# Performance work log

Hardware: AMD Instinct MI355X
Metric: run time of the kernel (lower is better)

## Reference

```python
import jax, jax.numpy as jnp
import numpy as np


def setup_inputs() -> dict:
    key = jax.random.key(0)
    ks = jax.random.split(key, 6)
    B, Tq, Tk = 4, 512, 512
    Q, K, C = 1024, 1024, 256
    query = jax.random.normal(ks[0], (B, Tq, Q), dtype=jnp.float32)
    kmat = jax.random.normal(ks[1], (B, Tk, K), dtype=jnp.float32)
    # Linear weights (torch nn.Linear stores [out, in]; we keep [in, out] for einsum)
    Wq = jax.random.normal(ks[2], (Q, C), dtype=jnp.float32) / np.sqrt(Q)
    Wk = jax.random.normal(ks[3], (K, C), dtype=jnp.float32) / np.sqrt(K)
    w_attn = jax.random.normal(ks[4], (C,), dtype=jnp.float32) / np.sqrt(C)
    b_attn = jax.random.normal(ks[5], (), dtype=jnp.float32) * 0.01
    return {"query": query, "key": kmat, "Wq": Wq, "Wk": Wk,
            "w_attn": w_attn, "b_attn": b_attn}


def reference(query, key, Wq, Wk, w_attn, b_attn):
    # Additive (Bahdanau) attention scores.
    # q2ctx: (B, Tq, C); k2ctx: (B, Tk, C)
    q2ctx = jnp.einsum('bqi,ic->bqc', query, Wq)
    k2ctx = jnp.einsum('bki,ic->bkc', key, Wk)
    # broadcast add -> (B, Tq, Tk, C), tanh, project to scalar and squeeze
    ctx = jnp.tanh(q2ctx[:, :, None, :] + k2ctx[:, None, :, :])
    scores = jnp.einsum('bqkc,c->bqk', ctx, w_attn) + b_attn
    return scores  # (B, Tq, Tk)
```

## Files before the change

### kernel.cpp

```cpp
#include <hip/hip_runtime.h>
#include <hip/hip_bf16.h>

#define M_ROWS 2048
#define KDIM   1024
#define CDIM   256
#define TQ     512
#define TK     512

#define GBM 64
#define GBN 32
#define CK  128

#define SCALE2LOG2E 2.8853900817779268f

typedef __attribute__((ext_vector_type(8))) short short8;
typedef __attribute__((ext_vector_type(8))) unsigned short ushort8;
typedef __attribute__((ext_vector_type(4))) float floatx4;
typedef __attribute__((ext_vector_type(2))) float f32x2;

__device__ __forceinline__ short2 cvt2(float x, float y) {
    __hip_bfloat162 h = __float22bfloat162_rn(make_float2(x, y));
    short2 r;
    __builtin_memcpy(&r, &h, sizeof(r));
    return r;
}
__device__ __forceinline__ unsigned short f2bf1(float x) {
    return (unsigned short)cvt2(x, x).x;
}
__device__ __forceinline__ float bf2f(unsigned short u) {
    return __builtin_bit_cast(float, (unsigned)u << 16);
}
__device__ __forceinline__ f32x2 splat2(float x) { return (f32x2){x, x}; }

__global__ __launch_bounds__(256) void gemm_mfma_kernel(
    const float* __restrict__ Aq, const float* __restrict__ Ak,
    const float* __restrict__ Wq, const float* __restrict__ Wk,
    const float* __restrict__ w_attn,
    unsigned short* __restrict__ Eq, unsigned short* __restrict__ Ek)
{
    __shared__ short Ws[GBN][CK + 8];

    const int z = blockIdx.z;
    const float* A = z ? Ak : Aq;
    const float* W = z ? Wk : Wq;
    unsigned short* E = z ? Ek : Eq;

    const int t    = threadIdx.x;
    const int lane = t & 63;
    const int wave = t >> 6;
    const int m0   = blockIdx.x * GBM;
    const int n0   = blockIdx.y * GBN;
    const int li   = lane & 15;
    const int qd   = lane >> 4;

    const int row = m0 + wave * 16 + li;
    const float* Arow = A + (size_t)row * KDIM + qd * 8;

    const int kr = t >> 1;
    const int h  = t & 1;
    const float* Wst = W + (size_t)kr * CDIM + n0 + h * 16;

    floatx4 acc0 = {0.f, 0.f, 0.f, 0.f};
    floatx4 acc1 = {0.f, 0.f, 0.f, 0.f};

    float4 wreg[4];
    #pragma unroll
    for (int u = 0; u < 4; ++u) wreg[u] = *(const float4*)&Wst[4 * u];

    for (int ck = 0; ck < KDIM / CK; ++ck) {
        __syncthreads();
        #pragma unroll
        for (int u = 0; u < 4; ++u) {
            short2 e0 = cvt2(wreg[u].x, wreg[u].y);
            short2 e1 = cvt2(wreg[u].z, wreg[u].w);
            const int c = h * 16 + 4 * u;
            Ws[c + 0][kr] = e0.x;
            Ws[c + 1][kr] = e0.y;
            Ws[c + 2][kr] = e1.x;
            Ws[c + 3][kr] = e1.y;
        }
        __syncthreads();
        if (ck + 1 < KDIM / CK) {
            const float* Wn = Wst + (size_t)(ck + 1) * CK * CDIM;
            #pragma unroll
            for (int u = 0; u < 4; ++u) wreg[u] = *(const float4*)&Wn[4 * u];
        }
        #pragma unroll
        for (int s = 0; s < 4; ++s) {
            const int kk = ck * CK + s * 32;
            float4 a0 = *(const float4*)&Arow[kk];
            float4 a1 = *(const float4*)&Arow[kk + 4];
            short8 af0 = *(const short8*)&Ws[li][s * 32 + qd * 8];
            short8 af1 = *(const short8*)&Ws[16 + li][s * 32 + qd * 8];
            short2 p0 = cvt2(a0.x, a0.y), p1 = cvt2(a0.z, a0.w);
            short2 p2 = cvt2(a1.x, a1.y), p3 = cvt2(a1.z, a1.w);
            short8 bv = { p0.x, p0.y, p1.x, p1.y, p2.x, p2.y, p3.x, p3.y };
            acc0 = __builtin_amdgcn_mfma_f32_16x16x32_bf16(af0, bv, acc0, 0, 0, 0);
            acc1 = __builtin_amdgcn_mfma_f32_16x16x32_bf16(af1, bv, acc1, 0, 0, 0);
        }
    }

    #pragma unroll
    for (int r = 0; r < 4; ++r) {
        const int c0 = n0 + qd * 4 + r;
        const int c1 = c0 + 16;
        float s0 = z ? 1.0f : (-0.5f / w_attn[c0]);
        float s1 = z ? 1.0f : (-0.5f / w_attn[c1]);
        float v0 = __builtin_amdgcn_exp2f(acc0[r] * SCALE2LOG2E) * s0;
        float v1 = __builtin_amdgcn_exp2f(acc1[r] * SCALE2LOG2E) * s1;
        E[(size_t)c0 * M_ROWS + row] = f2bf1(v0);
        E[(size_t)c1 * M_ROWS + row] = f2bf1(v1);
    }
}

__global__ __launch_bounds__(256) void bahdanau_kernel(
    const unsigned short* __restrict__ Eqs, const unsigned short* __restrict__ Ek,
    const float* __restrict__ w_attn, const float* __restrict__ b_attn,
    float* __restrict__ out)
{
    __shared__ float qs[64][36];
    __shared__ float ks[64][36];
    __shared__ __align__(16) float sl[CDIM];
    __shared__ float partial[4];

    const int t  = threadIdx.x;
    const int b  = blockIdx.z;
    const int q0 = blockIdx.x * 32;
    const int k0 = blockIdx.y * 32;
    const int gq = b * TQ + q0;
    const int gk = b * TK + k0;
    const int tq = (t >> 4) * 2;
    const int tk = (t & 15) * 2;

    const int lr = t >> 2;
    const int lc = (t & 3) * 8;

    {
        float wv = w_attn[t];
        sl[t] = -0.5f / wv;
        float sum = wv;
        #pragma unroll
        for (int o = 32; o >= 1; o >>= 1) sum += __shfl_down(sum, o);
        if ((t & 63) == 0) partial[t >> 6] = sum;
    }

    ushort8 qu = *(const ushort8*)&Eqs[(size_t)lr * M_ROWS + gq + lc];
    ushort8 ku = *(const ushort8*)&Ek [(size_t)lr * M_ROWS + gk + lc];

    f32x2 accA = {0.f, 0.f};
    f32x2 accB = {0.f, 0.f};

    for (int ch = 0; ch < 4; ++ch) {
        __syncthreads();
        *(float4*)&qs[lr][lc]     = make_float4(bf2f(qu[0]), bf2f(qu[1]), bf2f(qu[2]), bf2f(qu[3]));
        *(float4*)&qs[lr][lc + 4] = make_float4(bf2f(qu[4]), bf2f(qu[5]), bf2f(qu[6]), bf2f(qu[7]));
        *(float4*)&ks[lr][lc]     = make_float4(bf2f(ku[0]), bf2f(ku[1]), bf2f(ku[2]), bf2f(ku[3]));
        *(float4*)&ks[lr][lc + 4] = make_float4(bf2f(ku[4]), bf2f(ku[5]), bf2f(ku[6]), bf2f(ku[7]));
        __syncthreads();
        if (ch < 3) {
            const int c1 = (ch + 1) * 64;
            qu = *(const ushort8*)&Eqs[(size_t)(c1 + lr) * M_ROWS + gq + lc];
            ku = *(const ushort8*)&Ek [(size_t)(c1 + lr) * M_ROWS + gk + lc];
        }
        const int cb = ch * 64;
        #pragma unroll
        for (int cc = 0; cc < 64; cc += 4) {
            float4 s4 = *(const float4*)&sl[cb + cc];
            f32x2 q1 = *(const f32x2*)&qs[cc + 0][tq];
            f32x2 q2 = *(const f32x2*)&qs[cc + 1][tq];
            f32x2 q3 = *(const f32x2*)&qs[cc + 2][tq];
            f32x2 q4 = *(const f32x2*)&qs[cc + 3][tq];
            f32x2 k1 = *(const f32x2*)&ks[cc + 0][tk];
            f32x2 k2 = *(const f32x2*)&ks[cc + 1][tk];
            f32x2 k3 = *(const f32x2*)&ks[cc + 2][tk];
            f32x2 k4 = *(const f32x2*)&ks[cc + 3][tk];
            {
                f32x2 f1 = __builtin_elementwise_fma(splat2(q1.x), k1, splat2(s4.x));
                f32x2 f2 = __builtin_elementwise_fma(splat2(q2.x), k2, splat2(s4.y));
                f32x2 f3 = __builtin_elementwise_fma(splat2(q3.x), k3, splat2(s4.z));
                f32x2 f4 = __builtin_elementwise_fma(splat2(q4.x), k4, splat2(s4.w));
                f32x2 p12 = f1 * f2, p34 = f3 * f4;
                f32x2 s12 = f1 + f2, s34 = f3 + f4;
                f32x2 num = __builtin_elementwise_fma(s12, p34, s34 * p12);
                f32x2 den = p12 * p34;
                f32x2 r = {__builtin_amdgcn_rcpf(den.x), __builtin_amdgcn_rcpf(den.y)};
                accA = __builtin_elementwise_fma(num, r, accA);
            }
            {
                f32x2 f1 = __builtin_elementwise_fma(splat2(q1.y), k1, splat2(s4.x));
                f32x2 f2 = __builtin_elementwise_fma(splat2(q2.y), k2, splat2(s4.y));
                f32x2 f3 = __builtin_elementwise_fma(splat2(q3.y), k3, splat2(s4.z));
                f32x2 f4 = __builtin_elementwise_fma(splat2(q4.y), k4, splat2(s4.w));
                f32x2 p12 = f1 * f2, p34 = f3 * f4;
                f32x2 s12 = f1 + f2, s34 = f3 + f4;
                f32x2 num = __builtin_elementwise_fma(s12, p34, s34 * p12);
                f32x2 den = p12 * p34;
                f32x2 r = {__builtin_amdgcn_rcpf(den.x), __builtin_amdgcn_rcpf(den.y)};
                accB = __builtin_elementwise_fma(num, r, accB);
            }
        }
    }

    const float bias2 = *b_attn + partial[0] + partial[1] + partial[2] + partial[3];
    float* o = out + ((size_t)b * TQ + q0 + tq) * TK + k0 + tk;
    *(float2*)&o[0]  = make_float2(accA.x + bias2, accA.y + bias2);
    *(float2*)&o[TK] = make_float2(accB.x + bias2, accB.y + bias2);
}

extern "C" void kernel_launch(void* const* d_in, const int* in_sizes, int n_in,
                              void* d_out, int out_size, void* d_ws, size_t ws_size,
                              hipStream_t stream) {
    const float* query  = (const float*)d_in[0];
    const float* key    = (const float*)d_in[1];
    const float* Wq     = (const float*)d_in[2];
    const float* Wk     = (const float*)d_in[3];
    const float* w_attn = (const float*)d_in[4];
    const float* b_attn = (const float*)d_in[5];
    float* out = (float*)d_out;

    unsigned short* Eqs = (unsigned short*)d_ws;
    unsigned short* Ek  = Eqs + (size_t)CDIM * M_ROWS;

    dim3 gemm_grid(M_ROWS / GBM, CDIM / GBN, 2);
    gemm_mfma_kernel<<<gemm_grid, 256, 0, stream>>>(query, key, Wq, Wk, w_attn, Eqs, Ek);

    dim3 main_grid(TQ / 32, TK / 32, 4);
    bahdanau_kernel<<<main_grid, 256, 0, stream>>>(Eqs, Ek, w_attn, b_attn, out);
}
```

Baseline: 112.4 us.

## Stage full W tile in fragment-ordered LDS once, removing per-chunk barriers

The projection GEMM now loads the block's entire 1024x32 weight slice into LDS up front, converted to bf16 and stored in the exact MFMA fragment order. The K-loop then runs 32 steps with no __syncthreads and no register double-buffering of W. This removes the per-chunk barriers and the transposed scalar LDS stores. In exchange, the block uses 64KB of LDS, which may lower occupancy, and the whole weight load is serialized before any compute begins.

```diff
diff --git a/kernel.cpp b/kernel.cpp
--- a/kernel.cpp
+++ b/kernel.cpp
@@ -9,7 +9,6 @@
 
 #define GBM 64
 #define GBN 32
-#define CK  128
 
 #define SCALE2LOG2E 2.8853900817779268f
 
@@ -38,7 +37,7 @@
     const float* __restrict__ w_attn,
     unsigned short* __restrict__ Eq, unsigned short* __restrict__ Ek)
 {
-    __shared__ short Ws[GBN][CK + 8];
+    __shared__ short Wfrag[32 * 4 * GBN * 8];
 
     const int z = blockIdx.z;
     const float* A = z ? Ak : Aq;
@@ -53,51 +52,45 @@
     const int li   = lane & 15;
     const int qd   = lane >> 4;
 
+    {
+        const int sr = t >> 3;
+        const int sc = (t & 7) * 4;
+        const int jj = sr & 7;
+        const int fq = sr >> 3;
+        #pragma unroll 8
+        for (int p = 0; p < 32; ++p) {
+            const int k = p * 32 + sr;
+            float4 v = *(const float4*)&W[(size_t)k * CDIM + n0 + sc];
+            short2 e0 = cvt2(v.x, v.y);
+            short2 e1 = cvt2(v.z, v.w);
+            short* dst = &Wfrag[(((p * 4 + fq) * GBN) + sc) * 8 + jj];
+            dst[0]  = e0.x;
+            dst[8]  = e0.y;
+            dst[16] = e1.x;
+            dst[24] = e1.y;
+        }
+    }
+    __syncthreads();
+
     const int row = m0 + wave * 16 + li;
     const float* Arow = A + (size_t)row * KDIM + qd * 8;
-
-    const int kr = t >> 1;
-    const int h  = t & 1;
-    const float* Wst = W + (size_t)kr * CDIM + n0 + h * 16;
+    const short* wf0 = &Wfrag[(qd * GBN + li) * 8];
+    const short* wf1 = &Wfrag[(qd * GBN + 16 + li) * 8];
 
     floatx4 acc0 = {0.f, 0.f, 0.f, 0.f};
     floatx4 acc1 = {0.f, 0.f, 0.f, 0.f};
 
-    float4 wreg[4];
-    #pragma unroll
-    for (int u = 0; u < 4; ++u) wreg[u] = *(const float4*)&Wst[4 * u];
-
-    for (int ck = 0; ck < KDIM / CK; ++ck) {
-        __syncthreads();
-        #pragma unroll
-        for (int u = 0; u < 4; ++u) {
-            short2 e0 = cvt2(wreg[u].x, wreg[u].y);
-            short2 e1 = cvt2(wreg[u].z, wreg[u].w);
-            const int c = h * 16 + 4 * u;
-            Ws[c + 0][kr] = e0.x;
-            Ws[c + 1][kr] = e0.y;
-            Ws[c + 2][kr] = e1.x;
-            Ws[c + 3][kr] = e1.y;
-        }
-        __syncthreads();
-        if (ck + 1 < KDIM / CK) {
-            const float* Wn = Wst + (size_t)(ck + 1) * CK * CDIM;
-            #pragma unroll
-            for (int u = 0; u < 4; ++u) wreg[u] = *(const float4*)&Wn[4 * u];
-        }
-        #pragma unroll
-        for (int s = 0; s < 4; ++s) {
-            const int kk = ck * CK + s * 32;
-            float4 a0 = *(const float4*)&Arow[kk];
-            float4 a1 = *(const float4*)&Arow[kk + 4];
-            short8 af0 = *(const short8*)&Ws[li][s * 32 + qd * 8];
-            short8 af1 = *(const short8*)&Ws[16 + li][s * 32 + qd * 8];
-            short2 p0 = cvt2(a0.x, a0.y), p1 = cvt2(a0.z, a0.w);
-            short2 p2 = cvt2(a1.x, a1.y), p3 = cvt2(a1.z, a1.w);
-            short8 bv = { p0.x, p0.y, p1.x, p1.y, p2.x, p2.y, p3.x, p3.y };
-            acc0 = __builtin_amdgcn_mfma_f32_16x16x32_bf16(af0, bv, acc0, 0, 0, 0);
-            acc1 = __builtin_amdgcn_mfma_f32_16x16x32_bf16(af1, bv, acc1, 0, 0, 0);
-        }
+    #pragma unroll 8
+    for (int s = 0; s < 32; ++s) {
+        float4 a0 = *(const float4*)&Arow[s * 32];
+        float4 a1 = *(const float4*)&Arow[s * 32 + 4];
+        short8 af0 = *(const short8*)&wf0[s * 4 * GBN * 8];
+        short8 af1 = *(const short8*)&wf1[s * 4 * GBN * 8];
+        short2 p0 = cvt2(a0.x, a0.y), p1 = cvt2(a0.z, a0.w);
+        short2 p2 = cvt2(a1.x, a1.y), p3 = cvt2(a1.z, a1.w);
+        short8 bv = { p0.x, p0.y, p1.x, p1.y, p2.x, p2.y, p3.x, p3.y };
+        acc0 = __builtin_amdgcn_mfma_f32_16x16x32_bf16(af0, bv, acc0, 0, 0, 0);
+        acc1 = __builtin_amdgcn_mfma_f32_16x16x32_bf16(af1, bv, acc1, 0, 0, 0);
     }
 
     #pragma unroll
```

Measured after the change: 112.7 us. About the same (+0.3%).

## Fuse GEMM and Bahdanau kernels into one persistent launch with grid barrier

Applied to the files above, without the earlier changes.

Merges the projection GEMM kernel and the score kernel into a single launch of 1024 blocks. The first 512 blocks compute the exp-transformed projections, then every block waits on an atomic-counter grid barrier before computing its score tile, and the two stages share LDS through a union. The aim is to remove the second launch and the gap between kernels. In exchange it adds a memset, a spin barrier that needs all 1024 blocks co-resident to avoid deadlock, and idle time for the 512 blocks that skip the GEMM stage.

```diff
diff --git a/kernel.cpp b/kernel.cpp
--- a/kernel.cpp
+++ b/kernel.cpp
@@ -10,6 +10,7 @@
 #define GBM 64
 #define GBN 32
 #define CK  128
+#define NBLOCKS 1024u
 
 #define SCALE2LOG2E 2.8853900817779268f
 
@@ -32,101 +33,114 @@
 }
 __device__ __forceinline__ f32x2 splat2(float x) { return (f32x2){x, x}; }
 
-__global__ __launch_bounds__(256) void gemm_mfma_kernel(
+union SharedU {
+    short ws[GBN][CK + 8];
+    struct { float qs[64][36]; float ks[64][36]; } bah;
+};
+
+__global__ __launch_bounds__(256, 4) void fused_kernel(
     const float* __restrict__ Aq, const float* __restrict__ Ak,
     const float* __restrict__ Wq, const float* __restrict__ Wk,
-    const float* __restrict__ w_attn,
-    unsigned short* __restrict__ Eq, unsigned short* __restrict__ Ek)
+    const float* __restrict__ w_attn, const float* __restrict__ b_attn,
+    unsigned short* __restrict__ Eqs, unsigned short* __restrict__ Ek,
+    unsigned* __restrict__ counter, float* __restrict__ out)
 {
-    __shared__ short Ws[GBN][CK + 8];
-
-    const int z = blockIdx.z;
-    const float* A = z ? Ak : Aq;
-    const float* W = z ? Wk : Wq;
-    unsigned short* E = z ? Ek : Eq;
-
-    const int t    = threadIdx.x;
-    const int lane = t & 63;
-    const int wave = t >> 6;
-    const int m0   = blockIdx.x * GBM;
-    const int n0   = blockIdx.y * GBN;
-    const int li   = lane & 15;
-    const int qd   = lane >> 4;
-
-    const int row = m0 + wave * 16 + li;
-    const float* Arow = A + (size_t)row * KDIM + qd * 8;
-
-    const int kr = t >> 1;
-    const int h  = t & 1;
-    const float* Wst = W + (size_t)kr * CDIM + n0 + h * 16;
-
-    floatx4 acc0 = {0.f, 0.f, 0.f, 0.f};
-    floatx4 acc1 = {0.f, 0.f, 0.f, 0.f};
-
-    float4 wreg[4];
-    #pragma unroll
-    for (int u = 0; u < 4; ++u) wreg[u] = *(const float4*)&Wst[4 * u];
-
-    for (int ck = 0; ck < KDIM / CK; ++ck) {
-        __syncthreads();
-        #pragma unroll
-        for (int u = 0; u < 4; ++u) {
-            short2 e0 = cvt2(wreg[u].x, wreg[u].y);
-            short2 e1 = cvt2(wreg[u].z, wreg[u].w);
-            const int c = h * 16 + 4 * u;
-            Ws[c + 0][kr] = e0.x;
-            Ws[c + 1][kr] = e0.y;
-            Ws[c + 2][kr] = e1.x;
-            Ws[c + 3][kr] = e1.y;
-        }
-        __syncthreads();
-        if (ck + 1 < KDIM / CK) {
-            const float* Wn = Wst + (size_t)(ck + 1) * CK * CDIM;
-            #pragma unroll
-            for (int u = 0; u < 4; ++u) wreg[u] = *(const float4*)&Wn[4 * u];
-        }
-        #pragma unroll
-        for (int s = 0; s < 4; ++s) {
-            const int kk = ck * CK + s * 32;
-            float4 a0 = *(const float4*)&Arow[kk];
-            float4 a1 = *(const float4*)&Arow[kk + 4];
-            short8 af0 = *(const short8*)&Ws[li][s * 32 + qd * 8];
-            short8 af1 = *(const short8*)&Ws[16 + li][s * 32 + qd * 8];
-            short2 p0 = cvt2(a0.x, a0.y), p1 = cvt2(a0.z, a0.w);
-            short2 p2 = cvt2(a1.x, a1.y), p3 = cvt2(a1.z, a1.w);
-            short8 bv = { p0.x, p0.y, p1.x, p1.y, p2.x, p2.y, p3.x, p3.y };
-            acc0 = __builtin_amdgcn_mfma_f32_16x16x32_bf16(af0, bv, acc0, 0, 0, 0);
-            acc1 = __builtin_amdgcn_mfma_f32_16x16x32_bf16(af1, bv, acc1, 0, 0, 0);
-        }
-    }
-
-    #pragma unroll
-    for (int r = 0; r < 4; ++r) {
-        const int c0 = n0 + qd * 4 + r;
-        const int c1 = c0 + 16;
-        float s0 = z ? 1.0f : (-0.5f / w_attn[c0]);
-        float s1 = z ? 1.0f : (-0.5f / w_attn[c1]);
-        float v0 = __builtin_amdgcn_exp2f(acc0[r] * SCALE2LOG2E) * s0;
-        float v1 = __builtin_amdgcn_exp2f(acc1[r] * SCALE2LOG2E) * s1;
-        E[(size_t)c0 * M_ROWS + row] = f2bf1(v0);
-        E[(size_t)c1 * M_ROWS + row] = f2bf1(v1);
-    }
-}
-
-__global__ __launch_bounds__(256) void bahdanau_kernel(
-    const unsigned short* __restrict__ Eqs, const unsigned short* __restrict__ Ek,
-    const float* __restrict__ w_attn, const float* __restrict__ b_attn,
-    float* __restrict__ out)
-{
-    __shared__ float qs[64][36];
-    __shared__ float ks[64][36];
+    __shared__ SharedU sh;
     __shared__ __align__(16) float sl[CDIM];
     __shared__ float partial[4];
 
+    const int id = blockIdx.x;
     const int t  = threadIdx.x;
-    const int b  = blockIdx.z;
-    const int q0 = blockIdx.x * 32;
-    const int k0 = blockIdx.y * 32;
+
+    if (id < 512) {
+        const int z  = id >> 8;
+        const int by = (id >> 5) & 7;
+        const int bx = id & 31;
+        const float* A = z ? Ak : Aq;
+        const float* W = z ? Wk : Wq;
+        unsigned short* E = z ? Ek : Eqs;
+
+        const int lane = t & 63;
+        const int wave = t >> 6;
+        const int m0   = bx * GBM;
+        const int n0   = by * GBN;
+        const int li   = lane & 15;
+        const int qd   = lane >> 4;
+
+        const int row = m0 + wave * 16 + li;
+        const float* Arow = A + (size_t)row * KDIM + qd * 8;
+
+        const int kr = t >> 1;
+        const int h  = t & 1;
+        const float* Wst = W + (size_t)kr * CDIM + n0 + h * 16;
+
+        floatx4 acc0 = {0.f, 0.f, 0.f, 0.f};
+        floatx4 acc1 = {0.f, 0.f, 0.f, 0.f};
+
+        float4 wreg[4];
+        #pragma unroll
+        for (int u = 0; u < 4; ++u) wreg[u] = *(const float4*)&Wst[4 * u];
+
+        for (int ck = 0; ck < KDIM / CK; ++ck) {
+            __syncthreads();
+            #pragma unroll
+            for (int u = 0; u < 4; ++u) {
+                short2 e0 = cvt2(wreg[u].x, wreg[u].y);
+                short2 e1 = cvt2(wreg[u].z, wreg[u].w);
+                const int c = h * 16 + 4 * u;
+                sh.ws[c + 0][kr] = e0.x;
+                sh.ws[c + 1][kr] = e0.y;
+                sh.ws[c + 2][kr] = e1.x;
+                sh.ws[c + 3][kr] = e1.y;
+            }
+            __syncthreads();
+            if (ck + 1 < KDIM / CK) {
+                const float* Wn = Wst + (size_t)(ck + 1) * CK * CDIM;
+                #pragma unroll
+                for (int u = 0; u < 4; ++u) wreg[u] = *(const float4*)&Wn[4 * u];
+            }
+            #pragma unroll
+            for (int s = 0; s < 4; ++s) {
+                const int kk = ck * CK + s * 32;
+                float4 a0 = *(const float4*)&Arow[kk];
+                float4 a1 = *(const float4*)&Arow[kk + 4];
+                short8 af0 = *(const short8*)&sh.ws[li][s * 32 + qd * 8];
+                short8 af1 = *(const short8*)&sh.ws[16 + li][s * 32 + qd * 8];
+                short2 p0 = cvt2(a0.x, a0.y), p1 = cvt2(a0.z, a0.w);
+                short2 p2 = cvt2(a1.x, a1.y), p3 = cvt2(a1.z, a1.w);
+                short8 bv = { p0.x, p0.y, p1.x, p1.y, p2.x, p2.y, p3.x, p3.y };
+                acc0 = __builtin_amdgcn_mfma_f32_16x16x32_bf16(af0, bv, acc0, 0, 0, 0);
+                acc1 = __builtin_amdgcn_mfma_f32_16x16x32_bf16(af1, bv, acc1, 0, 0, 0);
+            }
+        }
+
+        #pragma unroll
+        for (int r = 0; r < 4; ++r) {
+            const int c0 = n0 + qd * 4 + r;
+            const int c1 = c0 + 16;
+            float s0 = z ? 1.0f : (-0.5f / w_attn[c0]);
+            float s1 = z ? 1.0f : (-0.5f / w_attn[c1]);
+            float v0 = __builtin_amdgcn_exp2f(acc0[r] * SCALE2LOG2E) * s0;
+            float v1 = __builtin_amdgcn_exp2f(acc1[r] * SCALE2LOG2E) * s1;
+            E[(size_t)c0 * M_ROWS + row] = f2bf1(v0);
+            E[(size_t)c1 * M_ROWS + row] = f2bf1(v1);
+        }
+    }
+
+    __syncthreads();
+    if (t == 0) {
+        __threadfence();
+        atomicAdd(counter, 1u);
+        while (atomicAdd(counter, 0u) < NBLOCKS) __builtin_amdgcn_s_sleep(2);
+        __threadfence();
+    }
+    __syncthreads();
+
+    const int qb = id & 15;
+    const int kb = (id >> 4) & 15;
+    const int b  = id >> 8;
+    const int q0 = qb * 32;
+    const int k0 = kb * 32;
     const int gq = b * TQ + q0;
     const int gk = b * TK + k0;
     const int tq = (t >> 4) * 2;
@@ -152,10 +166,10 @@
 
     for (int ch = 0; ch < 4; ++ch) {
         __syncthreads();
-        *(float4*)&qs[lr][lc]     = make_float4(bf2f(qu[0]), bf2f(qu[1]), bf2f(qu[2]), bf2f(qu[3]));
-        *(float4*)&qs[lr][lc + 4] = make_float4(bf2f(qu[4]), bf2f(qu[5]), bf2f(qu[6]), bf2f(qu[7]));
-        *(float4*)&ks[lr][lc]     = make_float4(bf2f(ku[0]), bf2f(ku[1]), bf2f(ku[2]), bf2f(ku[3]));
-        *(float4*)&ks[lr][lc + 4] = make_float4(bf2f(ku[4]), bf2f(ku[5]), bf2f(ku[6]), bf2f(ku[7]));
+        *(float4*)&sh.bah.qs[lr][lc]     = make_float4(bf2f(qu[0]), bf2f(qu[1]), bf2f(qu[2]), bf2f(qu[3]));
+        *(float4*)&sh.bah.qs[lr][lc + 4] = make_float4(bf2f(qu[4]), bf2f(qu[5]), bf2f(qu[6]), bf2f(qu[7]));
+        *(float4*)&sh.bah.ks[lr][lc]     = make_float4(bf2f(ku[0]), bf2f(ku[1]), bf2f(ku[2]), bf2f(ku[3]));
+        *(float4*)&sh.bah.ks[lr][lc + 4] = make_float4(bf2f(ku[4]), bf2f(ku[5]), bf2f(ku[6]), bf2f(ku[7]));
         __syncthreads();
         if (ch < 3) {
             const int c1 = (ch + 1) * 64;
@@ -166,14 +180,14 @@
         #pragma unroll
         for (int cc = 0; cc < 64; cc += 4) {
             float4 s4 = *(const float4*)&sl[cb + cc];
-            f32x2 q1 = *(const f32x2*)&qs[cc + 0][tq];
-            f32x2 q2 = *(const f32x2*)&qs[cc + 1][tq];
-            f32x2 q3 = *(const f32x2*)&qs[cc + 2][tq];
-            f32x2 q4 = *(const f32x2*)&qs[cc + 3][tq];
-            f32x2 k1 = *(const f32x2*)&ks[cc + 0][tk];
-            f32x2 k2 = *(const f32x2*)&ks[cc + 1][tk];
-            f32x2 k3 = *(const f32x2*)&ks[cc + 2][tk];
-            f32x2 k4 = *(const f32x2*)&ks[cc + 3][tk];
+            f32x2 q1 = *(const f32x2*)&sh.bah.qs[cc + 0][tq];
+            f32x2 q2 = *(const f32x2*)&sh.bah.qs[cc + 1][tq];
+            f32x2 q3 = *(const f32x2*)&sh.bah.qs[cc + 2][tq];
+            f32x2 q4 = *(const f32x2*)&sh.bah.qs[cc + 3][tq];
+            f32x2 k1 = *(const f32x2*)&sh.bah.ks[cc + 0][tk];
+            f32x2 k2 = *(const f32x2*)&sh.bah.ks[cc + 1][tk];
+            f32x2 k3 = *(const f32x2*)&sh.bah.ks[cc + 2][tk];
+            f32x2 k4 = *(const f32x2*)&sh.bah.ks[cc + 3][tk];
             {
                 f32x2 f1 = __builtin_elementwise_fma(splat2(q1.x), k1, splat2(s4.x));
                 f32x2 f2 = __builtin_elementwise_fma(splat2(q2.x), k2, splat2(s4.y));
@@ -220,10 +234,9 @@
 
     unsigned short* Eqs = (unsigned short*)d_ws;
     unsigned short* Ek  = Eqs + (size_t)CDIM * M_ROWS;
-
-    dim3 gemm_grid(M_ROWS / GBM, CDIM / GBN, 2);
-    gemm_mfma_kernel<<<gemm_grid, 256, 0, stream>>>(query, key, Wq, Wk, w_attn, Eqs, Ek);
-
-    dim3 main_grid(TQ / 32, TK / 32, 4);
-    bahdanau_kernel<<<main_grid, 256, 0, stream>>>(Eqs, Ek, w_attn, b_attn, out);
-}
+    unsigned* counter = (unsigned*)((char*)d_ws + (2u << 20));
+
+    hipMemsetAsync(counter, 0, sizeof(unsigned), stream);
+    fused_kernel<<<dim3(NBLOCKS), dim3(256), 0, stream>>>(
+        query, key, Wq, Wk, w_attn, b_attn, Eqs, Ek, counter, out);
+}
```

Result: slower. 231.7 us (+106.2%).
